# Optimization experiments

Measured on AMD Instinct MI355X. Metric: run time of the kernel, lower is better.

Reference implementation:

```python
import jax, jax.numpy as jnp
import numpy as np

HID, HEADS, HD = 512, 8, 64  # hid_dim, n_heads, head_dim
NEG = -1e10


def setup_inputs() -> dict:
    key = jax.random.key(0)
    ks = jax.random.split(key, 12)
    B, S = 4, 2048
    inp = {
        'query': jax.random.normal(ks[0], (B, S, HID), jnp.float32),
        'key': jax.random.normal(ks[1], (B, S, HID), jnp.float32),
        'value': jax.random.normal(ks[2], (B, S, HID), jnp.float32),
        'mask': jnp.ones((B, 1, 1, S), jnp.int32),
    }
    sc = 1.0 / np.sqrt(HID)
    for i, n in enumerate(['Wq', 'Wk', 'Wv', 'Wo']):
        inp[n] = jax.random.uniform(ks[3 + i], (HID, HID), jnp.float32, -sc, sc)
    for i, n in enumerate(['bq', 'bk', 'bv', 'bo']):
        inp[n] = jax.random.uniform(ks[7 + i], (HID,), jnp.float32, -sc, sc)
    return inp


def reference(query, key, value, mask, Wq, Wk, Wv, Wo, bq, bk, bv, bo):
    B = query.shape[0]

    def proj(x, W, b):
        # torch Linear: x @ W.T + b; then split heads -> [B, H, S, HD]
        y = jnp.einsum('bsd,ed->bse', x, W) + b
        return y.reshape(B, -1, HEADS, HD).transpose(0, 2, 1, 3)

    Q = proj(query, Wq, bq)
    K = proj(key, Wk, bk)
    V = proj(value, Wv, bv)
    scale = jnp.sqrt(jnp.float32(HD))
    E = jnp.einsum('bhqd,bhkd->bhqk', Q, K) / scale  # [B,H,Sq,Sk]
    E = jnp.where(mask == 0, NEG, E)
    A = jax.nn.softmax(E, axis=-1)  # dropout p=0 -> identity
    out = jnp.einsum('bhqk,bhkd->bhqd', A, V)
    out = out.transpose(0, 2, 1, 3).reshape(B, -1, HID)
    return jnp.einsum('bsd,ed->bse', out, Wo) + bo
```

## Files before the change

kernel.cpp:

```cpp
#include <hip/hip_runtime.h>
#include <hip/hip_bf16.h>


typedef __bf16 v8bf __attribute__((ext_vector_type(8)));
typedef __bf16 v4bf __attribute__((ext_vector_type(4)));
typedef float  v4f  __attribute__((ext_vector_type(4)));

#define MFMA16(a, b, c) __builtin_amdgcn_mfma_f32_16x16x32_bf16((a), (b), (c), 0, 0, 0)

__device__ inline v8bf cvt8(const float* __restrict__ p) {
    const v4f f0 = *(const v4f*)p;
    const v4f f1 = *(const v4f*)(p + 4);
    v8bf r;
    r[0] = (__bf16)f0[0]; r[1] = (__bf16)f0[1]; r[2] = (__bf16)f0[2]; r[3] = (__bf16)f0[3];
    r[4] = (__bf16)f1[0]; r[5] = (__bf16)f1[1]; r[6] = (__bf16)f1[2]; r[7] = (__bf16)f1[3];
    return r;
}

__global__ __launch_bounds__(256) void cvt_w(
    const float* __restrict__ Wq, const float* __restrict__ Wk,
    const float* __restrict__ Wv, const float* __restrict__ Wo,
    __bf16* __restrict__ out)
{
    const int idx = (blockIdx.x * 256 + threadIdx.x) * 4;
    const int w = idx >> 18, off = idx & 262143;
    const float* src = (w == 0) ? Wq : (w == 1) ? Wk : (w == 2) ? Wv : Wo;
    const v4f x = *(const v4f*)(src + off);
    v4bf y;
    y[0] = (__bf16)x[0]; y[1] = (__bf16)x[1]; y[2] = (__bf16)x[2]; y[3] = (__bf16)x[3];
    *(v4bf*)(out + idx) = y;
}

__global__ __launch_bounds__(256) void qkv_gemm(
    const float* __restrict__ xq, const float* __restrict__ xk, const float* __restrict__ xv,
    const __bf16* __restrict__ Wb,
    const float* __restrict__ bq, const float* __restrict__ bk, const float* __restrict__ bv,
    __bf16* __restrict__ Qo, __bf16* __restrict__ Ko, __bf16* __restrict__ VTo)
{
    const int z = blockIdx.z;
    const float*  x    = (z == 0) ? xq : (z == 1) ? xk : xv;
    const __bf16* W    = Wb + (size_t)z * 262144;
    const float*  bias = (z == 0) ? bq : (z == 1) ? bk : bv;

    const int tid = threadIdx.x, wave = tid >> 6, lane = tid & 63;
    const int quad = lane >> 4, r = lane & 15;
    const int wm = wave >> 1, wn = wave & 1;
    const int row0 = blockIdx.x * 128, col0 = blockIdx.y * 128;

    __shared__ __align__(16) __bf16 As[8192];
    __shared__ __align__(16) __bf16 Bs[8192];

    const float*  aptr[4];
    const __bf16* bptr[4];
    int adst[4], bdst[4];
    for (int j = 0; j < 4; j++) {
        const int e = tid + 256 * j;
        const int seg = e >> 6, ln = e & 63;
        aptr[j] = x + (size_t)(row0 + (seg >> 1) * 16 + (ln & 15)) * 512
                    + (seg & 1) * 32 + (ln >> 4) * 8;
        adst[j] = e * 8;
        const int segb = wave * 4 + j;
        bptr[j] = W + (size_t)(col0 + (segb >> 1) * 16 + r) * 512
                    + (segb & 1) * 32 + quad * 8;
        bdst[j] = (segb * 64 + lane) * 8;
    }

    v4f acc[4][4] = {};
    v8bf aReg[4], bReg[4];
    for (int j = 0; j < 4; j++) {
        aReg[j] = cvt8(aptr[j]);
        bReg[j] = *(const v8bf*)bptr[j];
    }

    for (int ki = 0; ki < 8; ki++) {
        __syncthreads();
        for (int j = 0; j < 4; j++) {
            *(v8bf*)&As[adst[j]] = aReg[j];
            *(v8bf*)&Bs[bdst[j]] = bReg[j];
        }
        __syncthreads();
        if (ki < 7) {
            const int kk = (ki + 1) * 64;
            for (int j = 0; j < 4; j++) {
                aReg[j] = cvt8(aptr[j] + kk);
                bReg[j] = *(const v8bf*)(bptr[j] + kk);
            }
        }
        for (int kc = 0; kc < 2; kc++) {
            v8bf a[4], b[4];
            for (int i = 0; i < 4; i++)
                a[i] = ((const v8bf*)As)[((wm * 4 + i) * 2 + kc) * 64 + lane];
            for (int i = 0; i < 4; i++)
                b[i] = ((const v8bf*)Bs)[((wn * 4 + i) * 2 + kc) * 64 + lane];
            for (int mi = 0; mi < 4; mi++)
                for (int ni = 0; ni < 4; ni++)
                    acc[mi][ni] = MFMA16(a[mi], b[ni], acc[mi][ni]);
        }
    }

    for (int ni = 0; ni < 4; ni++) {
        const int n = col0 + wn * 64 + ni * 16 + r;
        const float bv_ = bias[n];
        const int hh = n >> 6, hd = n & 63;
        for (int mi = 0; mi < 4; mi++) {
            const int mbase = row0 + wm * 64 + mi * 16 + quad * 4;
            const int bb = mbase >> 11, s0 = mbase & 2047;
            if (z == 2) {
                v4bf pk;
                for (int i = 0; i < 4; i++)
                    pk[i] = (__bf16)(acc[mi][ni][i] + bv_);
                *(v4bf*)&VTo[((size_t)((bb * 8 + hh) * 64 + hd)) * 2048 + s0] = pk;
            } else {
                __bf16* dst = (z == 0) ? Qo : Ko;
                for (int i = 0; i < 4; i++)
                    dst[((size_t)((bb * 8 + hh) * 2048 + s0 + i)) * 64 + hd] =
                        (__bf16)(acc[mi][ni][i] + bv_);
            }
        }
    }
}

__global__ __launch_bounds__(256, 2) void attn(
    const __bf16* __restrict__ Q, const __bf16* __restrict__ K,
    const __bf16* __restrict__ VT, const int* __restrict__ mask,
    __bf16* __restrict__ AO)
{
    const int id = blockIdx.y * 16 + blockIdx.x;
    const int x8 = id & 7, j = (id >> 3) & 3, qb = id >> 5;
    const int bh = x8 * 4 + j;
    const int b = bh >> 3, h = bh & 7;
    const int tid = threadIdx.x, wave = tid >> 6, lane = tid & 63;
    const int quad = lane >> 4, r = lane & 15;
    const int q0 = qb * 128 + wave * 32;

    const __bf16* Qb = Q  + (size_t)bh * 2048 * 64;
    const __bf16* Kb = K  + (size_t)bh * 2048 * 64;
    const __bf16* Vb = VT + (size_t)bh * 64 * 2048;
    const int*    mb = mask + (size_t)b * 2048;

    __shared__ __align__(16) __bf16 Kls[4096];
    __shared__ __align__(16) __bf16 Vls[4096];
    __shared__ __align__(16) float  biasF[2048];
    __shared__ __align__(16) __bf16 Pls[4][2][16][72];

    for (int i = tid; i < 2048; i += 256)
        biasF[i] = (mb[i] != 0) ? 0.f : -1.0e10f;

    const int e1 = tid, e2 = tid + 256;
    int seg, l, t_, h_, rr, qd;
    seg = e1 >> 6; l = e1 & 63; t_ = seg >> 1; h_ = seg & 1; rr = l & 15; qd = l >> 4;
    const __bf16* kg1 = Kb + (size_t)(16 * t_ + rr) * 64   + h_ * 32 + qd * 8;
    const __bf16* vg1 = Vb + (size_t)(16 * t_ + rr) * 2048 + h_ * 32 + qd * 8;
    seg = e2 >> 6; l = e2 & 63; t_ = seg >> 1; h_ = seg & 1; rr = l & 15; qd = l >> 4;
    const __bf16* kg2 = Kb + (size_t)(16 * t_ + rr) * 64   + h_ * 32 + qd * 8;
    const __bf16* vg2 = Vb + (size_t)(16 * t_ + rr) * 2048 + h_ * 32 + qd * 8;

    v8bf qf[2][2];
    for (int g = 0; g < 2; g++) {
        qf[g][0] = *(const v8bf*)(Qb + (size_t)(q0 + g * 16 + r) * 64 +      quad * 8);
        qf[g][1] = *(const v8bf*)(Qb + (size_t)(q0 + g * 16 + r) * 64 + 32 + quad * 8);
    }

    v8bf ones;
    for (int i = 0; i < 8; i++) ones[i] = (__bf16)1.0f;

    v4f o[2][4] = {};
    v4f osum[2] = {};

    const float SC = 0.18033688f;

    v8bf ks1 = *(const v8bf*)kg1, ks2 = *(const v8bf*)kg2;
    v8bf vs1 = *(const v8bf*)vg1, vs2 = *(const v8bf*)vg2;

    for (int t = 0; t < 32; t++) {
        __syncthreads();
        ((v8bf*)Kls)[e1] = ks1; ((v8bf*)Kls)[e2] = ks2;
        ((v8bf*)Vls)[e1] = vs1; ((v8bf*)Vls)[e2] = vs2;
        __syncthreads();
        if (t < 31) {
            const int k0n = (t + 1) * 64;
            ks1 = *(const v8bf*)(kg1 + (size_t)k0n * 64);
            ks2 = *(const v8bf*)(kg2 + (size_t)k0n * 64);
            vs1 = *(const v8bf*)(vg1 + k0n);
            vs2 = *(const v8bf*)(vg2 + k0n);
        }
        const int k0 = t * 64;

        v4f sa[2][4] = {};
        for (int tt = 0; tt < 4; tt++) {
            const v8bf kf0 = ((const v8bf*)Kls)[(tt * 2 + 0) * 64 + lane];
            const v8bf kf1 = ((const v8bf*)Kls)[(tt * 2 + 1) * 64 + lane];
            sa[0][tt] = MFMA16(kf0, qf[0][0], sa[0][tt]);
            sa[0][tt] = MFMA16(kf1, qf[0][1], sa[0][tt]);
            sa[1][tt] = MFMA16(kf0, qf[1][0], sa[1][tt]);
            sa[1][tt] = MFMA16(kf1, qf[1][1], sa[1][tt]);
        }

        for (int tt = 0; tt < 4; tt++) {
            const v4f bl = *(const v4f*)&biasF[k0 + tt * 16 + quad * 4];
            for (int g = 0; g < 2; g++) {
                v4bf pk;
                for (int i = 0; i < 4; i++) {
                    const float p = __builtin_amdgcn_exp2f(fmaf(sa[g][tt][i], SC, bl[i]));
                    pk[i] = (__bf16)p;
                }
                *(v4bf*)&Pls[wave][g][r][tt * 16 + quad * 4] = pk;
            }
        }
        asm volatile("s_waitcnt lgkmcnt(0)" ::: "memory");
        v8bf pa[2][2];
        for (int g = 0; g < 2; g++) {
            pa[g][0] = *(const v8bf*)&Pls[wave][g][r][     quad * 8];
            pa[g][1] = *(const v8bf*)&Pls[wave][g][r][32 + quad * 8];
        }

        osum[0] = MFMA16(pa[0][0], ones, osum[0]);
        osum[0] = MFMA16(pa[0][1], ones, osum[0]);
        osum[1] = MFMA16(pa[1][0], ones, osum[1]);
        osum[1] = MFMA16(pa[1][1], ones, osum[1]);

        for (int t2 = 0; t2 < 4; t2++) {
            const v8bf vf0 = ((const v8bf*)Vls)[(t2 * 2 + 0) * 64 + lane];
            const v8bf vf1 = ((const v8bf*)Vls)[(t2 * 2 + 1) * 64 + lane];
            o[0][t2] = MFMA16(pa[0][0], vf0, o[0][t2]);
            o[0][t2] = MFMA16(pa[0][1], vf1, o[0][t2]);
            o[1][t2] = MFMA16(pa[1][0], vf0, o[1][t2]);
            o[1][t2] = MFMA16(pa[1][1], vf1, o[1][t2]);
        }
    }

    for (int g = 0; g < 2; g++) {
        float inv[4];
        for (int i = 0; i < 4; i++) inv[i] = 1.0f / osum[g][i];
        for (int t2 = 0; t2 < 4; t2++) {
            const int hd = t2 * 16 + r;
            for (int i = 0; i < 4; i++) {
                const int s = q0 + g * 16 + quad * 4 + i;
                AO[((size_t)b * 2048 + s) * 512 + h * 64 + hd] =
                    (__bf16)(o[g][t2][i] * inv[i]);
            }
        }
    }
}

__global__ __launch_bounds__(256) void out_gemm(
    const __bf16* __restrict__ Ai, const __bf16* __restrict__ W,
    const float* __restrict__ bias, float* __restrict__ y)
{
    const int tid = threadIdx.x, wave = tid >> 6, lane = tid & 63;
    const int quad = lane >> 4, r = lane & 15;
    const int wm = wave >> 1, wn = wave & 1;
    const int row0 = blockIdx.x * 128, col0 = blockIdx.y * 128;

    __shared__ __align__(16) __bf16 As[8192];
    __shared__ __align__(16) __bf16 Bs[8192];

    const __bf16* aptr[4];
    const __bf16* bptr[4];
    int dst_[4];
    for (int j = 0; j < 4; j++) {
        const int segb = wave * 4 + j;
        aptr[j] = Ai + (size_t)(row0 + (segb >> 1) * 16 + r) * 512 + (segb & 1) * 32 + quad * 8;
        bptr[j] = W  + (size_t)(col0 + (segb >> 1) * 16 + r) * 512 + (segb & 1) * 32 + quad * 8;
        dst_[j] = (segb * 64 + lane) * 8;
    }

    v4f acc[4][4] = {};
    v8bf aReg[4], bReg[4];
    for (int j = 0; j < 4; j++) {
        aReg[j] = *(const v8bf*)aptr[j];
        bReg[j] = *(const v8bf*)bptr[j];
    }

    for (int ki = 0; ki < 8; ki++) {
        __syncthreads();
        for (int j = 0; j < 4; j++) {
            *(v8bf*)&As[dst_[j]] = aReg[j];
            *(v8bf*)&Bs[dst_[j]] = bReg[j];
        }
        __syncthreads();
        if (ki < 7) {
            const int kk = (ki + 1) * 64;
            for (int j = 0; j < 4; j++) {
                aReg[j] = *(const v8bf*)(aptr[j] + kk);
                bReg[j] = *(const v8bf*)(bptr[j] + kk);
            }
        }
        for (int kc = 0; kc < 2; kc++) {
            v8bf a[4], b[4];
            for (int i = 0; i < 4; i++)
                a[i] = ((const v8bf*)As)[((wm * 4 + i) * 2 + kc) * 64 + lane];
            for (int i = 0; i < 4; i++)
                b[i] = ((const v8bf*)Bs)[((wn * 4 + i) * 2 + kc) * 64 + lane];
            for (int mi = 0; mi < 4; mi++)
                for (int ni = 0; ni < 4; ni++)
                    acc[mi][ni] = MFMA16(a[mi], b[ni], acc[mi][ni]);
        }
    }

    for (int ni = 0; ni < 4; ni++) {
        const int n = col0 + wn * 64 + ni * 16 + r;
        const float bv_ = bias[n];
        for (int mi = 0; mi < 4; mi++) {
            const int mbase = row0 + wm * 64 + mi * 16 + quad * 4;
            for (int i = 0; i < 4; i++)
                y[(size_t)(mbase + i) * 512 + n] = acc[mi][ni][i] + bv_;
        }
    }
}

extern "C" void kernel_launch(void* const* d_in, const int* in_sizes, int n_in,
                              void* d_out, int out_size, void* d_ws, size_t ws_size,
                              hipStream_t stream)
{
    const float* q    = (const float*)d_in[0];
    const float* k    = (const float*)d_in[1];
    const float* v    = (const float*)d_in[2];
    const int*   mask = (const int*)d_in[3];
    const float* Wq   = (const float*)d_in[4];
    const float* Wk   = (const float*)d_in[5];
    const float* Wv   = (const float*)d_in[6];
    const float* Wo   = (const float*)d_in[7];
    const float* bq   = (const float*)d_in[8];
    const float* bk   = (const float*)d_in[9];
    const float* bv   = (const float*)d_in[10];
    const float* bo   = (const float*)d_in[11];

    __bf16* ws  = (__bf16*)d_ws;
    __bf16* Qw  = ws;
    __bf16* Kw  = ws + 4194304;
    __bf16* VTw = ws + 8388608;
    __bf16* AOw = ws + 12582912;
    __bf16* Wb  = ws + 16777216;

    cvt_w<<<dim3(1024), 256, 0, stream>>>(Wq, Wk, Wv, Wo, Wb);
    qkv_gemm<<<dim3(64, 4, 3), 256, 0, stream>>>(q, k, v, Wb, bq, bk, bv, Qw, Kw, VTw);
    attn<<<dim3(16, 32), 256, 0, stream>>>(Qw, Kw, VTw, mask, AOw);
    out_gemm<<<dim3(64, 4), 256, 0, stream>>>(AOw, Wb + 786432, bo, (float*)d_out);
}
```

Baseline: 220.1 us.

## Pre-convert inputs to bf16 and use direct global-to-LDS loads in GEMMs

Adds a separate kernel that converts the fp32 query/key/value activations to bf16 in workspace, so the QKV GEMM can stage tiles with global_load_lds straight into shared memory instead of going through registers. The out-projection GEMM also switches to global_load_lds and halves its M tile to 64 rows, doubling the grid for better occupancy. This removes register staging but also drops the previous register prefetch overlap, so each k-step now waits on its load. The extra conversion pass adds a full read and write of the inputs through HBM.

```diff
diff --git a/kernel.cpp b/kernel.cpp
--- a/kernel.cpp
+++ b/kernel.cpp
@@ -7,6 +7,12 @@
 typedef float  v4f  __attribute__((ext_vector_type(4)));
 
 #define MFMA16(a, b, c) __builtin_amdgcn_mfma_f32_16x16x32_bf16((a), (b), (c), 0, 0, 0)
+
+__device__ __forceinline__ void gl16(const __bf16* g, __bf16* l) {
+    __builtin_amdgcn_global_load_lds(
+        (const __attribute__((address_space(1))) void*)g,
+        (__attribute__((address_space(3))) void*)l, 16, 0, 0);
+}
 
 __device__ inline v8bf cvt8(const float* __restrict__ p) {
     const v4f f0 = *(const v4f*)p;
@@ -31,14 +37,23 @@
     *(v4bf*)(out + idx) = y;
 }
 
+__global__ __launch_bounds__(256) void cvt_x(
+    const float* __restrict__ xq, const float* __restrict__ xk,
+    const float* __restrict__ xv, __bf16* __restrict__ out)
+{
+    const int idx = (blockIdx.x * 256 + threadIdx.x) * 8;
+    const int w = idx >> 22, off = idx & 4194303;
+    const float* src = (w == 0) ? xq : (w == 1) ? xk : xv;
+    *(v8bf*)(out + idx) = cvt8(src + off);
+}
+
 __global__ __launch_bounds__(256) void qkv_gemm(
-    const float* __restrict__ xq, const float* __restrict__ xk, const float* __restrict__ xv,
-    const __bf16* __restrict__ Wb,
+    const __bf16* __restrict__ xb, const __bf16* __restrict__ Wb,
     const float* __restrict__ bq, const float* __restrict__ bk, const float* __restrict__ bv,
     __bf16* __restrict__ Qo, __bf16* __restrict__ Ko, __bf16* __restrict__ VTo)
 {
     const int z = blockIdx.z;
-    const float*  x    = (z == 0) ? xq : (z == 1) ? xk : xv;
+    const __bf16* x    = xb + (size_t)z * 4194304;
     const __bf16* W    = Wb + (size_t)z * 262144;
     const float*  bias = (z == 0) ? bq : (z == 1) ? bk : bv;
 
@@ -50,42 +65,28 @@
     __shared__ __align__(16) __bf16 As[8192];
     __shared__ __align__(16) __bf16 Bs[8192];
 
-    const float*  aptr[4];
-    const __bf16* bptr[4];
-    int adst[4], bdst[4];
+    const __bf16* aG[4];
+    const __bf16* bG[4];
+    __bf16* aL[4];
+    __bf16* bL[4];
     for (int j = 0; j < 4; j++) {
-        const int e = tid + 256 * j;
-        const int seg = e >> 6, ln = e & 63;
-        aptr[j] = x + (size_t)(row0 + (seg >> 1) * 16 + (ln & 15)) * 512
-                    + (seg & 1) * 32 + (ln >> 4) * 8;
-        adst[j] = e * 8;
-        const int segb = wave * 4 + j;
-        bptr[j] = W + (size_t)(col0 + (segb >> 1) * 16 + r) * 512
-                    + (segb & 1) * 32 + quad * 8;
-        bdst[j] = (segb * 64 + lane) * 8;
+        const int s = wave * 4 + j;
+        aG[j] = x + (size_t)(row0 + (s >> 1) * 16 + r) * 512 + (s & 1) * 32 + quad * 8;
+        bG[j] = W + (size_t)(col0 + (s >> 1) * 16 + r) * 512 + (s & 1) * 32 + quad * 8;
+        aL[j] = &As[s * 512];
+        bL[j] = &Bs[s * 512];
     }
 
     v4f acc[4][4] = {};
-    v8bf aReg[4], bReg[4];
-    for (int j = 0; j < 4; j++) {
-        aReg[j] = cvt8(aptr[j]);
-        bReg[j] = *(const v8bf*)bptr[j];
-    }
 
     for (int ki = 0; ki < 8; ki++) {
+        const int kk = ki * 64;
         __syncthreads();
         for (int j = 0; j < 4; j++) {
-            *(v8bf*)&As[adst[j]] = aReg[j];
-            *(v8bf*)&Bs[bdst[j]] = bReg[j];
-        }
-        __syncthreads();
-        if (ki < 7) {
-            const int kk = (ki + 1) * 64;
-            for (int j = 0; j < 4; j++) {
-                aReg[j] = cvt8(aptr[j] + kk);
-                bReg[j] = *(const v8bf*)(bptr[j] + kk);
-            }
-        }
+            gl16(aG[j] + kk, aL[j]);
+            gl16(bG[j] + kk, bL[j]);
+        }
+        __syncthreads();
         for (int kc = 0; kc < 2; kc++) {
             v8bf a[4], b[4];
             for (int i = 0; i < 4; i++)
@@ -250,49 +251,43 @@
     const int tid = threadIdx.x, wave = tid >> 6, lane = tid & 63;
     const int quad = lane >> 4, r = lane & 15;
     const int wm = wave >> 1, wn = wave & 1;
-    const int row0 = blockIdx.x * 128, col0 = blockIdx.y * 128;
-
-    __shared__ __align__(16) __bf16 As[8192];
+    const int row0 = blockIdx.x * 64, col0 = blockIdx.y * 128;
+
+    __shared__ __align__(16) __bf16 As[4096];
     __shared__ __align__(16) __bf16 Bs[8192];
 
-    const __bf16* aptr[4];
-    const __bf16* bptr[4];
-    int dst_[4];
+    const __bf16* aG[2];
+    const __bf16* bG[4];
+    __bf16* aL[2];
+    __bf16* bL[4];
+    for (int j = 0; j < 2; j++) {
+        const int s = wave * 2 + j;
+        aG[j] = Ai + (size_t)(row0 + (s >> 1) * 16 + r) * 512 + (s & 1) * 32 + quad * 8;
+        aL[j] = &As[s * 512];
+    }
     for (int j = 0; j < 4; j++) {
-        const int segb = wave * 4 + j;
-        aptr[j] = Ai + (size_t)(row0 + (segb >> 1) * 16 + r) * 512 + (segb & 1) * 32 + quad * 8;
-        bptr[j] = W  + (size_t)(col0 + (segb >> 1) * 16 + r) * 512 + (segb & 1) * 32 + quad * 8;
-        dst_[j] = (segb * 64 + lane) * 8;
-    }
-
-    v4f acc[4][4] = {};
-    v8bf aReg[4], bReg[4];
-    for (int j = 0; j < 4; j++) {
-        aReg[j] = *(const v8bf*)aptr[j];
-        bReg[j] = *(const v8bf*)bptr[j];
-    }
+        const int s = wave * 4 + j;
+        bG[j] = W + (size_t)(col0 + (s >> 1) * 16 + r) * 512 + (s & 1) * 32 + quad * 8;
+        bL[j] = &Bs[s * 512];
+    }
+
+    v4f acc[2][4] = {};
 
     for (int ki = 0; ki < 8; ki++) {
-        __syncthreads();
-        for (int j = 0; j < 4; j++) {
-            *(v8bf*)&As[dst_[j]] = aReg[j];
-            *(v8bf*)&Bs[dst_[j]] = bReg[j];
-        }
-        __syncthreads();
-        if (ki < 7) {
-            const int kk = (ki + 1) * 64;
-            for (int j = 0; j < 4; j++) {
-                aReg[j] = *(const v8bf*)(aptr[j] + kk);
-                bReg[j] = *(const v8bf*)(bptr[j] + kk);
-            }
-        }
+        const int kk = ki * 64;
+        __syncthreads();
+        gl16(aG[0] + kk, aL[0]);
+        gl16(aG[1] + kk, aL[1]);
+        for (int j = 0; j < 4; j++)
+            gl16(bG[j] + kk, bL[j]);
+        __syncthreads();
         for (int kc = 0; kc < 2; kc++) {
-            v8bf a[4], b[4];
-            for (int i = 0; i < 4; i++)
-                a[i] = ((const v8bf*)As)[((wm * 4 + i) * 2 + kc) * 64 + lane];
+            v8bf a[2], b[4];
+            for (int i = 0; i < 2; i++)
+                a[i] = ((const v8bf*)As)[((wm * 2 + i) * 2 + kc) * 64 + lane];
             for (int i = 0; i < 4; i++)
                 b[i] = ((const v8bf*)Bs)[((wn * 4 + i) * 2 + kc) * 64 + lane];
-            for (int mi = 0; mi < 4; mi++)
+            for (int mi = 0; mi < 2; mi++)
                 for (int ni = 0; ni < 4; ni++)
                     acc[mi][ni] = MFMA16(a[mi], b[ni], acc[mi][ni]);
         }
@@ -301,8 +296,8 @@
     for (int ni = 0; ni < 4; ni++) {
         const int n = col0 + wn * 64 + ni * 16 + r;
         const float bv_ = bias[n];
-        for (int mi = 0; mi < 4; mi++) {
-            const int mbase = row0 + wm * 64 + mi * 16 + quad * 4;
+        for (int mi = 0; mi < 2; mi++) {
+            const int mbase = row0 + wm * 32 + mi * 16 + quad * 4;
             for (int i = 0; i < 4; i++)
                 y[(size_t)(mbase + i) * 512 + n] = acc[mi][ni][i] + bv_;
         }
@@ -332,9 +327,11 @@
     __bf16* VTw = ws + 8388608;
     __bf16* AOw = ws + 12582912;
     __bf16* Wb  = ws + 16777216;
+    __bf16* xbw = ws + 17825792;
 
     cvt_w<<<dim3(1024), 256, 0, stream>>>(Wq, Wk, Wv, Wo, Wb);
-    qkv_gemm<<<dim3(64, 4, 3), 256, 0, stream>>>(q, k, v, Wb, bq, bk, bv, Qw, Kw, VTw);
+    cvt_x<<<dim3(6144), 256, 0, stream>>>(q, k, v, xbw);
+    qkv_gemm<<<dim3(64, 4, 3), 256, 0, stream>>>(xbw, Wb, bq, bk, bv, Qw, Kw, VTw);
     attn<<<dim3(16, 32), 256, 0, stream>>>(Qw, Kw, VTw, mask, AOw);
-    out_gemm<<<dim3(64, 4), 256, 0, stream>>>(AOw, Wb + 786432, bo, (float*)d_out);
-}
+    out_gemm<<<dim3(128, 4), 256, 0, stream>>>(AOw, Wb + 786432, bo, (float*)d_out);
+}
```

New measurement: 206.9 us. 1.06x faster.
